# Optimization experiments

Hardware: AMD Instinct MI355X
Metric: run time of the kernel (lower is better)

The kernel has to match this reference:

```python
import jax, jax.numpy as jnp
import numpy as np

N, D, K = 200000, 128, 512


def setup_inputs() -> dict:
    key = jax.random.key(0)
    F = jax.random.normal(key, (N, D), dtype=jnp.float32)
    # original picks starting centers as (unique) rows of F; take a strided subset
    centers = F[:: N // K][:K]
    return {"F": F, "centers": centers}


def reference(F, centers):
    # One k-means iteration (the original's aliasing bug makes the recursion
    # terminate after a single assignment + mean-update pass).
    # invariant to the sqrt the original applies.
    f2 = jnp.sum(F * F, axis=1, keepdims=True)          # [N,1]
    c2 = jnp.sum(centers * centers, axis=1)             # [K]
    d2 = f2 - 2.0 * (F @ centers.T) + c2[None, :]       # [N,K]
    assign = jnp.argmin(d2, axis=1)                      # [N] cluster index per point
    sums = jax.ops.segment_sum(F, assign, num_segments=K)                 # [K,D]
    counts = jax.ops.segment_sum(jnp.ones((F.shape[0],), F.dtype), assign,
                                 num_segments=K)                           # [K]
    new_centers = sums / jnp.maximum(counts, 1.0)[:, None]                 # segment mean
    return new_centers, assign
```

## Files before the change

kernel.cpp:

```cpp
#include <hip/hip_runtime.h>

#define DIM 128
#define K_CL 512
#define BM 128
#define CC 128
#define GAPU 4352u
#define TAU2 0.02f
#define LISTA_CAP 65536
#define LISTB_CAP 16384
#define TILE 1024
#define MAX_ITEMS 2048
#define G_GATHER 1024

typedef unsigned int uint;
typedef unsigned short ushort;
using short8 = __attribute__((ext_vector_type(8))) short;
using f32x4  = __attribute__((ext_vector_type(4))) float;
using us8    = __attribute__((ext_vector_type(8))) unsigned short;

__device__ __forceinline__ ushort f2bf(float x) {
    uint u = __float_as_uint(x);
    u += 0x7fff + ((u >> 16) & 1);
    return (ushort)(u >> 16);
}
__device__ __forceinline__ float bf2f(ushort h) {
    return __uint_as_float(((uint)h) << 16);
}
__device__ __forceinline__ uint umn(uint a, uint b) { return a < b ? a : b; }
__device__ __forceinline__ uint umx(uint a, uint b) { return a > b ? a : b; }

__device__ __forceinline__ void gload_lds16(const void* gsrc, void* ldst) {
    __builtin_amdgcn_global_load_lds(
        (const __attribute__((address_space(1))) unsigned int*)gsrc,
        (__attribute__((address_space(3))) unsigned int*)ldst,
        16, 0, 0);
}

__global__ void prep_kernel(const float* __restrict__ C, ushort* __restrict__ Cp,
                            float* __restrict__ c2, float* __restrict__ c2q,
                            double* __restrict__ c2d) {
    int bid = blockIdx.x;
    if (bid < 256) {
        int e = bid * 256 + threadIdx.x;
        int p = e >> 7, d = e & 127;
        float x = C[e];
        ushort h = f2bf(x);
        float lo = x - bf2f(h);
        Cp[(size_t)p * 256 + d] = h;
        Cp[(size_t)p * 256 + 128 + d] = f2bf(lo);
    } else {
        int k = (bid - 256) * 256 + threadIdx.x;
        if (k < K_CL) {
            const float* row = C + (size_t)k * DIM;
            float s = 0.f;
            double sd = 0.0;
            for (int d = 0; d < DIM; ++d) {
                s = fmaf(row[d], row[d], s);
                double v = (double)row[d];
                sd += v * v;
            }
            c2[k] = s;
            c2q[k] = s + 3072.0f;
            c2d[k] = sd;
        }
    }
}

__global__ __launch_bounds__(256, 2)
void assign_hi(const float* __restrict__ F, const ushort* __restrict__ Cp,
               const float* __restrict__ c2qg, float* __restrict__ assign_out,
               int* __restrict__ cntA, int* __restrict__ listA,
               int* __restrict__ cntB, int* __restrict__ listB, int N) {
    __shared__ __align__(16) ushort Fs[BM * 128];
    __shared__ __align__(16) ushort Cs[128 * 128];

    const int tid  = threadIdx.x;
    const int lane = tid & 63;
    const int wave = tid >> 6;
    const int quad = lane >> 4;
    const int l15  = lane & 15;
    const int wy   = wave >> 1;
    const int wx   = wave & 1;
    const int p0   = blockIdx.x * BM;

#pragma unroll
    for (int t = 0; t < 8; ++t) {
        int G = tid + 256 * t;
        int r = G >> 4, pos = G & 15;
        int g = (pos & 8) | ((pos ^ r) & 7);
        int gp = p0 + r; if (gp >= N) gp = N - 1;
        const float* src = F + (size_t)gp * DIM + g * 8;
        float4 x0 = ((const float4*)src)[0];
        float4 x1 = ((const float4*)src)[1];
        us8 o;
        o[0] = f2bf(x0.x); o[1] = f2bf(x0.y); o[2] = f2bf(x0.z); o[3] = f2bf(x0.w);
        o[4] = f2bf(x1.x); o[5] = f2bf(x1.y); o[6] = f2bf(x1.z); o[7] = f2bf(x1.w);
        *((us8*)&Fs[(size_t)G * 8]) = o;
    }

    int prA[4], xA[4], cnB[4], xB[4];
#pragma unroll
    for (int i = 0; i < 4; ++i) {
        int pr = wy * 64 + i * 16 + l15;
        prA[i] = pr * 128; xA[i] = quad ^ (pr & 7);
    }
#pragma unroll
    for (int j = 0; j < 4; ++j) {
        int cn = wx * 64 + j * 16 + l15;
        cnB[j] = cn * 128; xB[j] = quad ^ (cn & 7);
    }
    int csrc[8];
#pragma unroll
    for (int t = 0; t < 8; ++t) {
        int G = t * 256 + wave * 64 + lane;
        int r = G >> 4, pos = G & 15;
        int g = (pos & 8) | ((pos ^ r) & 7);
        csrc[t] = r * 256 + g * 8;
    }
    float c2q[4][4];
    uint  kb [4][4];
#pragma unroll
    for (int cc = 0; cc < 4; ++cc)
#pragma unroll
        for (int j = 0; j < 4; ++j) {
            int k = cc * CC + wx * 64 + j * 16 + l15;
            c2q[cc][j] = c2qg[k];
            kb [cc][j] = (uint)k;
        }

    uint m1[16], m2[16];
#pragma unroll
    for (int i = 0; i < 16; ++i) { m1[i] = 0xFFFFFFFFu; m2[i] = 0xFFFFFFFFu; }

#pragma unroll 1
    for (int cc = 0; cc < 4; ++cc) {
        f32x4 acc[4][4];
#pragma unroll
        for (int i = 0; i < 4; ++i)
#pragma unroll
            for (int j = 0; j < 4; ++j) acc[i][j] = f32x4{0.f, 0.f, 0.f, 0.f};

        __syncthreads();
#pragma unroll
        for (int t = 0; t < 8; ++t)
            gload_lds16(Cp + (size_t)cc * CC * 256 + csrc[t],
                        &Cs[(size_t)(t * 256 + wave * 64) * 8]);
        __syncthreads();

#pragma unroll
        for (int s = 0; s < 4; ++s) {
            const int hs = (s & 2) << 2;
            const int ls = (s & 1) << 2;
            short8 a[4], b[4];
#pragma unroll
            for (int j = 0; j < 4; ++j)
                b[j] = *((const short8*)&Cs[cnB[j] + (hs | (xB[j] ^ ls)) * 8]);
#pragma unroll
            for (int i = 0; i < 4; ++i)
                a[i] = *((const short8*)&Fs[prA[i] + (hs | (xA[i] ^ ls)) * 8]);
#pragma unroll
            for (int i = 0; i < 4; ++i)
#pragma unroll
                for (int j = 0; j < 4; ++j)
                    acc[i][j] = __builtin_amdgcn_mfma_f32_16x16x32_bf16(
                        a[i], b[j], acc[i][j], 0, 0, 0);
        }

#pragma unroll
        for (int i = 0; i < 4; ++i)
#pragma unroll
            for (int reg = 0; reg < 4; ++reg) {
                int lr = i * 4 + reg;
#pragma unroll
                for (int j = 0; j < 4; ++j) {
                    float dq = fmaf(acc[i][j][reg], -2.0f, c2q[cc][j]);
                    uint x = (__float_as_uint(dq) & 0xFFFFFE00u) | kb[cc][j];
                    uint t = umx(x, m1[lr]);
                    m2[lr] = umn(m2[lr], t);
                    m1[lr] = umn(m1[lr], x);
                }
            }
    }

#pragma unroll
    for (int lr = 0; lr < 16; ++lr) {
        uint a1 = m1[lr], a2 = m2[lr];
#pragma unroll
        for (int m = 1; m <= 8; m <<= 1) {
            uint o1 = (uint)__shfl_xor((int)a1, m);
            uint o2 = (uint)__shfl_xor((int)a2, m);
            uint hi = umx(a1, o1);
            a1 = umn(a1, o1);
            a2 = umn(umn(a2, o2), hi);
        }
        m1[lr] = a1; m2[lr] = a2;
    }

    __syncthreads();
    uint* sm1 = (uint*)Cs;
    uint* sm2 = sm1 + 256;

    if (l15 == 0) {
#pragma unroll
        for (int lr = 0; lr < 16; ++lr) {
            int pl = wy * 64 + (lr >> 2) * 16 + quad * 4 + (lr & 3);
            sm1[wx * 128 + pl] = m1[lr];
            sm2[wx * 128 + pl] = m2[lr];
        }
    }
    __syncthreads();

    if (tid < BM) {
        int p = p0 + tid;
        if (p < N) {
            uint a1 = sm1[tid], a2 = sm2[tid];
            uint b1 = sm1[128 + tid], b2 = sm2[128 + tid];
            uint hi = umx(a1, b1);
            uint M1 = umn(a1, b1);
            uint M2 = umn(umn(a2, b2), hi);
            assign_out[p] = (float)(M1 & 511u);
            if ((M2 & 0xFFFFFE00u) - (M1 & 0xFFFFFE00u) < GAPU) {
                int idx = atomicAdd(cntA, 1);
                if (idx < LISTA_CAP) listA[idx] = p;
                else {
                    int ib = atomicAdd(cntB, 1);
                    if (ib < LISTB_CAP) listB[ib] = p;
                }
            }
        }
    }
}

__global__ __launch_bounds__(256, 2)
void assign_lohi(const float* __restrict__ F, const ushort* __restrict__ Cp,
                 const float* __restrict__ c2g, float* __restrict__ assign_out,
                 const int* __restrict__ cntA, const int* __restrict__ listA,
                 int* __restrict__ cntB, int* __restrict__ listB, int N) {
    int cnt = *cntA; if (cnt > LISTA_CAP) cnt = LISTA_CAP;
    const int p0 = blockIdx.x * BM;
    if (p0 >= cnt) return;

    __shared__ __align__(16) ushort Fs[BM * 256];
    __shared__ __align__(16) ushort Cs[CC * 64];

    const int tid  = threadIdx.x;
    const int lane = tid & 63;
    const int wave = tid >> 6;
    const int quad = lane >> 4;
    const int l15  = lane & 15;
    const int wy   = wave >> 1;
    const int wx   = wave & 1;

    for (int G = tid; G < BM * 32; G += 256) {
        int r = G >> 5, pos = G & 31;
        int g = (pos & 24) | ((pos ^ r) & 7);
        int idx = p0 + r; if (idx >= cnt) idx = cnt - 1;
        int gp = listA[idx];
        const float* src = F + (size_t)gp * DIM + (g & 15) * 8;
        float4 x0 = ((const float4*)src)[0];
        float4 x1 = ((const float4*)src)[1];
        float xs[8] = {x0.x, x0.y, x0.z, x0.w, x1.x, x1.y, x1.z, x1.w};
        us8 o;
        if (g < 16) {
#pragma unroll
            for (int t = 0; t < 8; ++t) o[t] = f2bf(xs[t]);
        } else {
#pragma unroll
            for (int t = 0; t < 8; ++t) {
                ushort h = f2bf(xs[t]);
                o[t] = f2bf(xs[t] - bf2f(h));
            }
        }
        *((us8*)&Fs[(size_t)G * 8]) = o;
    }

    int aoff[4][2], boff[4][2];
#pragma unroll
    for (int i = 0; i < 4; ++i) {
        int pr = wy * 64 + i * 16 + l15;
#pragma unroll
        for (int s = 0; s < 2; ++s)
            aoff[i][s] = pr * 256 + (((s * 4 + quad) ^ (pr & 7)) * 8);
    }
#pragma unroll
    for (int j = 0; j < 4; ++j) {
        int cn = wx * 64 + j * 16 + l15;
#pragma unroll
        for (int s = 0; s < 2; ++s)
            boff[j][s] = cn * 64 + (((s * 4 + quad) ^ (cn & 7)) * 8);
    }
    int cpoff[4];
    ushort* ldsdst[4];
#pragma unroll
    for (int t = 0; t < 4; ++t) {
        int Gbase = t * 256 + wave * 64;
        int G = Gbase + lane;
        int r = G >> 3, pos = G & 7;
        int g = pos ^ (r & 7);
        cpoff[t] = r * 256 + g * 8;
        ldsdst[t] = &Cs[(size_t)Gbase * 8];
    }

    float best1[16], best2[16];
    int bidx[16];
#pragma unroll
    for (int i = 0; i < 16; ++i) { best1[i] = 3.4e38f; best2[i] = 3.4e38f; bidx[i] = 0; }

    for (int cc = 0; cc < K_CL / CC; ++cc) {
        const int ccbase = cc * (CC * 256);
        f32x4 acc[4][4];
#pragma unroll
        for (int i = 0; i < 4; ++i)
#pragma unroll
            for (int j = 0; j < 4; ++j) acc[i][j] = f32x4{0.f, 0.f, 0.f, 0.f};

#pragma unroll
        for (int st = 0; st < 4; ++st) {
            const int ak0 = st & 1;
            const int ak1 = (st < 2) ? (st + 2) : -1;

            __syncthreads();
#pragma unroll
            for (int t = 0; t < 4; ++t)
                gload_lds16(Cp + ccbase + st * 64 + cpoff[t], ldsdst[t]);
            __syncthreads();

#pragma unroll
            for (int s = 0; s < 2; ++s) {
                short8 b[4], a[4];
#pragma unroll
                for (int j = 0; j < 4; ++j)
                    b[j] = *((const short8*)&Cs[boff[j][s]]);
#pragma unroll
                for (int i = 0; i < 4; ++i)
                    a[i] = *((const short8*)&Fs[aoff[i][s] + ak0 * 64]);
#pragma unroll
                for (int i = 0; i < 4; ++i)
#pragma unroll
                    for (int j = 0; j < 4; ++j)
                        acc[i][j] = __builtin_amdgcn_mfma_f32_16x16x32_bf16(
                            a[i], b[j], acc[i][j], 0, 0, 0);
                if (ak1 >= 0) {
#pragma unroll
                    for (int i = 0; i < 4; ++i)
                        a[i] = *((const short8*)&Fs[aoff[i][s] + ak1 * 64]);
#pragma unroll
                    for (int i = 0; i < 4; ++i)
#pragma unroll
                        for (int j = 0; j < 4; ++j)
                            acc[i][j] = __builtin_amdgcn_mfma_f32_16x16x32_bf16(
                                a[i], b[j], acc[i][j], 0, 0, 0);
                }
            }
        }

        float c2v[4];
#pragma unroll
        for (int j = 0; j < 4; ++j)
            c2v[j] = c2g[cc * CC + wx * 64 + j * 16 + l15];
#pragma unroll
        for (int i = 0; i < 4; ++i)
#pragma unroll
            for (int reg = 0; reg < 4; ++reg) {
                int lr = i * 4 + reg;
#pragma unroll
                for (int j = 0; j < 4; ++j) {
                    float d = c2v[j] - 2.0f * acc[i][j][reg];
                    int k = cc * CC + wx * 64 + j * 16 + l15;
                    if (d < best1[lr]) { best2[lr] = best1[lr]; best1[lr] = d; bidx[lr] = k; }
                    else if (d < best2[lr]) best2[lr] = d;
                }
            }
    }

    __syncthreads();
    float* sb1 = (float*)Cs;
    float* sb2 = sb1 + 256;
    int*   sk  = (int*)(sb2 + 256);

#pragma unroll
    for (int lr = 0; lr < 16; ++lr) {
        float b1 = best1[lr], b2 = best2[lr];
        int k1 = bidx[lr];
#pragma unroll
        for (int m = 1; m <= 8; m <<= 1) {
            float ob1 = __shfl_xor(b1, m);
            float ob2 = __shfl_xor(b2, m);
            int   ok1 = __shfl_xor(k1, m);
            float nb2 = fminf(fmaxf(b1, ob1), fminf(b2, ob2));
            if (ob1 < b1 || (ob1 == b1 && ok1 < k1)) { b1 = ob1; k1 = ok1; }
            b2 = nb2;
        }
        best1[lr] = b1; best2[lr] = b2; bidx[lr] = k1;
    }
    if (l15 == 0) {
#pragma unroll
        for (int lr = 0; lr < 16; ++lr) {
            int pl = wy * 64 + (lr >> 2) * 16 + quad * 4 + (lr & 3);
            sb1[wx * 128 + pl] = best1[lr];
            sb2[wx * 128 + pl] = best2[lr];
            sk [wx * 128 + pl] = bidx[lr];
        }
    }
    __syncthreads();

    if (tid < BM && p0 + tid < cnt) {
        int p = listA[p0 + tid];
        float a1 = sb1[tid],       a2 = sb2[tid];        int akk = sk[tid];
        float c1 = sb1[128 + tid], cs2 = sb2[128 + tid]; int ckk = sk[128 + tid];
        float m2v = fminf(fmaxf(a1, c1), fminf(a2, cs2));
        float m1v; int mk;
        if (c1 < a1 || (c1 == a1 && ckk < akk)) { m1v = c1; mk = ckk; }
        else                                    { m1v = a1; mk = akk; }
        assign_out[p] = (float)mk;
        if (m2v - m1v < TAU2) {
            int ib = atomicAdd(cntB, 1);
            if (ib < LISTB_CAP) listB[ib] = p;
        }
    }
}

__global__ void rescue_kernel(const float* __restrict__ F, const float* __restrict__ C,
                              const double* __restrict__ c2d,
                              const int* __restrict__ cntB,
                              const int* __restrict__ listB,
                              float* __restrict__ assign_out) {
    __shared__ double Frow[DIM];
    __shared__ double bd[256];
    __shared__ int    bk[256];
    int cnt = *cntB;
    if (cnt > LISTB_CAP) cnt = LISTB_CAP;
    for (int r = blockIdx.x; r < cnt; r += gridDim.x) {
        int p = listB[r];
        if (threadIdx.x < DIM) Frow[threadIdx.x] = (double)F[(size_t)p * DIM + threadIdx.x];
        __syncthreads();
        double b1 = 1e300; int k1 = 0x7fffffff;
        for (int k = threadIdx.x; k < K_CL; k += 256) {
            const float* c = C + (size_t)k * DIM;
            double acc = 0.0;
            for (int d = 0; d < DIM; ++d) acc += Frow[d] * (double)c[d];
            double dd = c2d[k] - 2.0 * acc;
            if (dd < b1 || (dd == b1 && k < k1)) { b1 = dd; k1 = k; }
        }
        bd[threadIdx.x] = b1; bk[threadIdx.x] = k1;
        __syncthreads();
        for (int s = 128; s > 0; s >>= 1) {
            if (threadIdx.x < s) {
                double ob = bd[threadIdx.x + s]; int ok = bk[threadIdx.x + s];
                if (ob < bd[threadIdx.x] || (ob == bd[threadIdx.x] && ok < bk[threadIdx.x])) {
                    bd[threadIdx.x] = ob; bk[threadIdx.x] = ok;
                }
            }
            __syncthreads();
        }
        if (threadIdx.x == 0) assign_out[p] = (float)bk[0];
        __syncthreads();
    }
}

__global__ void count_kernel(const float* __restrict__ assign_f,
                             int* __restrict__ gcount, int N) {
    __shared__ int h[K_CL];
    const int tid = threadIdx.x;
    h[tid] = 0; h[tid + 256] = 0;
    __syncthreads();
    int base = blockIdx.x * 1024;
#pragma unroll
    for (int t = 0; t < 4; ++t) {
        int p = base + tid + t * 256;
        if (p < N) atomicAdd(&h[(int)assign_f[p]], 1);
    }
    __syncthreads();
#pragma unroll
    for (int t = 0; t < 2; ++t) {
        int k = tid + t * 256;
        if (h[k]) atomicAdd(&gcount[k], h[k]);
    }
}

__global__ void scan_item_kernel(const int* __restrict__ gcount,
                                 int* __restrict__ offsets, int* __restrict__ cursor,
                                 int* __restrict__ items, int* __restrict__ itemCnt,
                                 int N) {
    __shared__ int s[K_CL];
    __shared__ int ic;
    int t = threadIdx.x;
    int v = gcount[t];
    s[t] = v;
    if (t == 0) ic = 0;
    __syncthreads();
    for (int off = 1; off < K_CL; off <<= 1) {
        int x = (t >= off) ? s[t - off] : 0;
        __syncthreads();
        s[t] += x;
        __syncthreads();
    }
    offsets[t] = s[t] - v;
    cursor[t]  = s[t] - v;
    if (t == K_CL - 1) offsets[K_CL] = N;
    int nIt = (v + TILE - 1) / TILE;
    int base = 0;
    if (nIt > 0) base = atomicAdd(&ic, nIt);
    for (int i = 0; i < nIt; ++i)
        if (base + i < MAX_ITEMS) items[base + i] = (t << 8) | i;
    __syncthreads();
    if (t == 0) *itemCnt = ic < MAX_ITEMS ? ic : MAX_ITEMS;
}

__global__ void scatter_kernel(const float* __restrict__ assign_f,
                               int* __restrict__ cursor, int* __restrict__ idx, int N) {
    __shared__ int h[K_CL];
    __shared__ int b[K_CL];
    const int tid = threadIdx.x;
    h[tid] = 0; h[tid + 256] = 0;
    __syncthreads();
    int base = blockIdx.x * 1024;
    int a[4], r[4];
#pragma unroll
    for (int t = 0; t < 4; ++t) {
        int p = base + tid + t * 256;
        if (p < N) {
            a[t] = (int)assign_f[p];
            r[t] = atomicAdd(&h[a[t]], 1);
        } else a[t] = -1;
    }
    __syncthreads();
#pragma unroll
    for (int t = 0; t < 2; ++t) {
        int k = tid + t * 256;
        if (h[k]) b[k] = atomicAdd(&cursor[k], h[k]);
    }
    __syncthreads();
#pragma unroll
    for (int t = 0; t < 4; ++t) {
        if (a[t] >= 0) {
            int p = base + tid + t * 256;
            idx[b[a[t]] + r[t]] = p;
        }
    }
}

__global__ __launch_bounds__(256)
void gather_kernel(const float* __restrict__ F, const int* __restrict__ idx,
                   const int* __restrict__ offsets, const int* __restrict__ items,
                   const int* __restrict__ itemCnt, float* __restrict__ sums) {
    __shared__ int lidx[TILE];
    const int bid = blockIdx.x;
    if (bid >= *itemCnt) return;
    const int it    = items[bid];
    const int k     = it >> 8;
    const int chunk = it & 255;
    const int s   = offsets[k] + chunk * TILE;
    int e = offsets[k + 1];
    if (e > s + TILE) e = s + TILE;
    const int len = e - s;

    const int tid = threadIdx.x;
    for (int i = tid; i < len; i += 256) lidx[i] = idx[s + i];
    __syncthreads();

    const int d  = tid & 127;
    const int rg = tid >> 7;
    float acc = 0.f;
    for (int m0 = rg * 8; m0 < len; m0 += 16) {
        float v[8]; int ok[8];
#pragma unroll
        for (int t = 0; t < 8; ++t) {
            int m = m0 + t;
            ok[t] = (m < len);
            int p = lidx[ok[t] ? m : 0];
            v[t] = F[(size_t)p * DIM + d];
        }
#pragma unroll
        for (int t = 0; t < 8; ++t)
            if (ok[t]) acc += v[t];
    }
    unsafeAtomicAdd(&sums[(size_t)k * DIM + d], acc);
}

__global__ void finalize_kernel(const float* __restrict__ sums,
                                const int* __restrict__ gcount,
                                float* __restrict__ out) {
    int i = blockIdx.x * 256 + threadIdx.x;
    int k = i >> 7;
    out[i] = sums[i] / fmaxf((float)gcount[k], 1.0f);
}

extern "C" void kernel_launch(void* const* d_in, const int* in_sizes, int n_in,
                              void* d_out, int out_size, void* d_ws, size_t ws_size,
                              hipStream_t stream) {
    const float* F = (const float*)d_in[0];
    const float* C = (const float*)d_in[1];
    int N = in_sizes[0] / DIM;

    float* out = (float*)d_out;
    float* centers_out = out;
    float* assign_out  = out + K_CL * DIM;

    float*  sums    = (float*)d_ws;
    int*    gcount  = (int*)(sums + K_CL * DIM);
    int*    cursor  = gcount + K_CL;
    int*    offsets = cursor + K_CL;
    int*    itemCnt = offsets + 516;
    int*    cntA    = itemCnt + 4;
    int*    cntB    = cntA + 1;
    int*    items   = cntA + 8;
    int*    listA   = items + MAX_ITEMS;
    int*    listB   = listA + LISTA_CAP;
    float*  c2      = (float*)(listB + LISTB_CAP);
    float*  c2q     = c2 + K_CL;
    double* c2d     = (double*)(c2q + K_CL);
    ushort* Cp      = (ushort*)(c2d + K_CL);
    int*    idx     = (int*)(Cp + K_CL * 256);

    hipMemsetAsync(d_ws, 0,
                   (size_t)(K_CL * DIM) * sizeof(float) +
                   (512 + 512 + 516 + 4 + 8) * sizeof(int), stream);

    prep_kernel<<<258, 256, 0, stream>>>(C, Cp, c2, c2q, c2d);

    int nb = (N + BM - 1) / BM;
    assign_hi<<<nb, 256, 0, stream>>>(F, Cp, c2q, assign_out, cntA, listA, cntB, listB, N);

    assign_lohi<<<LISTA_CAP / BM, 256, 0, stream>>>(F, Cp, c2, assign_out,
                                                    cntA, listA, cntB, listB, N);

    rescue_kernel<<<256, 256, 0, stream>>>(F, C, c2d, cntB, listB, assign_out);

    int cb = (N + 1023) / 1024;
    count_kernel    <<<cb, 256, 0, stream>>>(assign_out, gcount, N);
    scan_item_kernel<<<1, K_CL, 0, stream>>>(gcount, offsets, cursor, items, itemCnt, N);
    scatter_kernel  <<<cb, 256, 0, stream>>>(assign_out, cursor, idx, N);
    gather_kernel   <<<G_GATHER, 256, 0, stream>>>(F, idx, offsets, items, itemCnt, sums);
    finalize_kernel <<<K_CL * DIM / 256, 256, 0, stream>>>(sums, gcount, centers_out);
}
```

Baseline: 336.8 us.

## Fuse cluster counting into assign kernels, widen assign_hi to 512 threads, restage lohi centers

assign_hi now runs 512-thread blocks with eight waves splitting the center columns four ways, which lowers per-thread accumulator registers and raises occupancy. It also builds a per-block shared histogram of assignments and flushes it to global counts. The lohi and rescue passes adjust those counts with atomics whenever they change an assignment, so the separate count kernel is removed. assign_lohi loads a full 128-center chunk into shared memory once per chunk instead of four staged loads with barriers. This costs more LDS per block and adds global atomics in the refinement kernels.

```diff
diff --git a/kernel.cpp b/kernel.cpp
--- a/kernel.cpp
+++ b/kernel.cpp
@@ -66,26 +66,30 @@
     }
 }
 
-__global__ __launch_bounds__(256, 2)
+__global__ __launch_bounds__(512, 4)
 void assign_hi(const float* __restrict__ F, const ushort* __restrict__ Cp,
                const float* __restrict__ c2qg, float* __restrict__ assign_out,
                int* __restrict__ cntA, int* __restrict__ listA,
-               int* __restrict__ cntB, int* __restrict__ listB, int N) {
+               int* __restrict__ cntB, int* __restrict__ listB,
+               int* __restrict__ gcount, int N) {
     __shared__ __align__(16) ushort Fs[BM * 128];
     __shared__ __align__(16) ushort Cs[128 * 128];
+    __shared__ int hist[K_CL];
 
     const int tid  = threadIdx.x;
     const int lane = tid & 63;
     const int wave = tid >> 6;
     const int quad = lane >> 4;
     const int l15  = lane & 15;
-    const int wy   = wave >> 1;
-    const int wx   = wave & 1;
+    const int wy   = wave & 1;
+    const int wq   = wave >> 1;
     const int p0   = blockIdx.x * BM;
 
-#pragma unroll
-    for (int t = 0; t < 8; ++t) {
-        int G = tid + 256 * t;
+    hist[tid] = 0;
+
+#pragma unroll
+    for (int t = 0; t < 4; ++t) {
+        int G = tid + 512 * t;
         int r = G >> 4, pos = G & 15;
         int g = (pos & 8) | ((pos ^ r) & 7);
         int gp = p0 + r; if (gp >= N) gp = N - 1;
@@ -98,35 +102,32 @@
         *((us8*)&Fs[(size_t)G * 8]) = o;
     }
 
-    int prA[4], xA[4], cnB[4], xB[4];
+    int prA[4], xA[4], cnB[2], xB[2];
 #pragma unroll
     for (int i = 0; i < 4; ++i) {
         int pr = wy * 64 + i * 16 + l15;
         prA[i] = pr * 128; xA[i] = quad ^ (pr & 7);
     }
 #pragma unroll
-    for (int j = 0; j < 4; ++j) {
-        int cn = wx * 64 + j * 16 + l15;
+    for (int j = 0; j < 2; ++j) {
+        int cn = wq * 32 + j * 16 + l15;
         cnB[j] = cn * 128; xB[j] = quad ^ (cn & 7);
     }
-    int csrc[8];
-#pragma unroll
-    for (int t = 0; t < 8; ++t) {
-        int G = t * 256 + wave * 64 + lane;
+    int csrc[4];
+#pragma unroll
+    for (int t = 0; t < 4; ++t) {
+        int G = t * 512 + wave * 64 + lane;
         int r = G >> 4, pos = G & 15;
         int g = (pos & 8) | ((pos ^ r) & 7);
         csrc[t] = r * 256 + g * 8;
     }
-    float c2q[4][4];
-    uint  kb [4][4];
+    const int kq = wq * 32 + l15;
+    float c2q[4][2];
 #pragma unroll
     for (int cc = 0; cc < 4; ++cc)
 #pragma unroll
-        for (int j = 0; j < 4; ++j) {
-            int k = cc * CC + wx * 64 + j * 16 + l15;
-            c2q[cc][j] = c2qg[k];
-            kb [cc][j] = (uint)k;
-        }
+        for (int j = 0; j < 2; ++j)
+            c2q[cc][j] = c2qg[cc * CC + kq + j * 16];
 
     uint m1[16], m2[16];
 #pragma unroll
@@ -134,26 +135,26 @@
 
 #pragma unroll 1
     for (int cc = 0; cc < 4; ++cc) {
-        f32x4 acc[4][4];
+        f32x4 acc[4][2];
 #pragma unroll
         for (int i = 0; i < 4; ++i)
 #pragma unroll
-            for (int j = 0; j < 4; ++j) acc[i][j] = f32x4{0.f, 0.f, 0.f, 0.f};
-
-        __syncthreads();
-#pragma unroll
-        for (int t = 0; t < 8; ++t)
+            for (int j = 0; j < 2; ++j) acc[i][j] = f32x4{0.f, 0.f, 0.f, 0.f};
+
+        __syncthreads();
+#pragma unroll
+        for (int t = 0; t < 4; ++t)
             gload_lds16(Cp + (size_t)cc * CC * 256 + csrc[t],
-                        &Cs[(size_t)(t * 256 + wave * 64) * 8]);
+                        &Cs[(size_t)(t * 512 + wave * 64) * 8]);
         __syncthreads();
 
 #pragma unroll
         for (int s = 0; s < 4; ++s) {
             const int hs = (s & 2) << 2;
             const int ls = (s & 1) << 2;
-            short8 a[4], b[4];
-#pragma unroll
-            for (int j = 0; j < 4; ++j)
+            short8 a[4], b[2];
+#pragma unroll
+            for (int j = 0; j < 2; ++j)
                 b[j] = *((const short8*)&Cs[cnB[j] + (hs | (xB[j] ^ ls)) * 8]);
 #pragma unroll
             for (int i = 0; i < 4; ++i)
@@ -161,7 +162,7 @@
 #pragma unroll
             for (int i = 0; i < 4; ++i)
 #pragma unroll
-                for (int j = 0; j < 4; ++j)
+                for (int j = 0; j < 2; ++j)
                     acc[i][j] = __builtin_amdgcn_mfma_f32_16x16x32_bf16(
                         a[i], b[j], acc[i][j], 0, 0, 0);
         }
@@ -172,9 +173,10 @@
             for (int reg = 0; reg < 4; ++reg) {
                 int lr = i * 4 + reg;
 #pragma unroll
-                for (int j = 0; j < 4; ++j) {
+                for (int j = 0; j < 2; ++j) {
                     float dq = fmaf(acc[i][j][reg], -2.0f, c2q[cc][j]);
-                    uint x = (__float_as_uint(dq) & 0xFFFFFE00u) | kb[cc][j];
+                    uint x = (__float_as_uint(dq) & 0xFFFFFE00u)
+                             | (uint)(cc * CC + kq + j * 16);
                     uint t = umx(x, m1[lr]);
                     m2[lr] = umn(m2[lr], t);
                     m1[lr] = umn(m1[lr], x);
@@ -198,14 +200,14 @@
 
     __syncthreads();
     uint* sm1 = (uint*)Cs;
-    uint* sm2 = sm1 + 256;
+    uint* sm2 = sm1 + 512;
 
     if (l15 == 0) {
 #pragma unroll
         for (int lr = 0; lr < 16; ++lr) {
             int pl = wy * 64 + (lr >> 2) * 16 + quad * 4 + (lr & 3);
-            sm1[wx * 128 + pl] = m1[lr];
-            sm2[wx * 128 + pl] = m2[lr];
+            sm1[wq * 128 + pl] = m1[lr];
+            sm2[wq * 128 + pl] = m2[lr];
         }
     }
     __syncthreads();
@@ -213,12 +215,17 @@
     if (tid < BM) {
         int p = p0 + tid;
         if (p < N) {
-            uint a1 = sm1[tid], a2 = sm2[tid];
-            uint b1 = sm1[128 + tid], b2 = sm2[128 + tid];
-            uint hi = umx(a1, b1);
-            uint M1 = umn(a1, b1);
-            uint M2 = umn(umn(a2, b2), hi);
-            assign_out[p] = (float)(M1 & 511u);
+            uint M1 = sm1[tid], M2 = sm2[tid];
+#pragma unroll
+            for (int q = 1; q < 4; ++q) {
+                uint b1 = sm1[q * 128 + tid], b2 = sm2[q * 128 + tid];
+                uint hi = umx(M1, b1);
+                M1 = umn(M1, b1);
+                M2 = umn(umn(M2, b2), hi);
+            }
+            int k = (int)(M1 & 511u);
+            assign_out[p] = (float)k;
+            atomicAdd(&hist[k], 1);
             if ((M2 & 0xFFFFFE00u) - (M1 & 0xFFFFFE00u) < GAPU) {
                 int idx = atomicAdd(cntA, 1);
                 if (idx < LISTA_CAP) listA[idx] = p;
@@ -229,19 +236,22 @@
             }
         }
     }
-}
-
-__global__ __launch_bounds__(256, 2)
+    __syncthreads();
+    { int v = hist[tid]; if (v) atomicAdd(&gcount[tid], v); }
+}
+
+__global__ __launch_bounds__(256, 1)
 void assign_lohi(const float* __restrict__ F, const ushort* __restrict__ Cp,
                  const float* __restrict__ c2g, float* __restrict__ assign_out,
                  const int* __restrict__ cntA, const int* __restrict__ listA,
-                 int* __restrict__ cntB, int* __restrict__ listB, int N) {
+                 int* __restrict__ cntB, int* __restrict__ listB,
+                 int* __restrict__ gcount, int N) {
     int cnt = *cntA; if (cnt > LISTA_CAP) cnt = LISTA_CAP;
     const int p0 = blockIdx.x * BM;
     if (p0 >= cnt) return;
 
     __shared__ __align__(16) ushort Fs[BM * 256];
-    __shared__ __align__(16) ushort Cs[CC * 64];
+    __shared__ __align__(16) ushort Cs[CC * 256];
 
     const int tid  = threadIdx.x;
     const int lane = tid & 63;
@@ -287,18 +297,7 @@
         int cn = wx * 64 + j * 16 + l15;
 #pragma unroll
         for (int s = 0; s < 2; ++s)
-            boff[j][s] = cn * 64 + (((s * 4 + quad) ^ (cn & 7)) * 8);
-    }
-    int cpoff[4];
-    ushort* ldsdst[4];
-#pragma unroll
-    for (int t = 0; t < 4; ++t) {
-        int Gbase = t * 256 + wave * 64;
-        int G = Gbase + lane;
-        int r = G >> 3, pos = G & 7;
-        int g = pos ^ (r & 7);
-        cpoff[t] = r * 256 + g * 8;
-        ldsdst[t] = &Cs[(size_t)Gbase * 8];
+            boff[j][s] = cn * 256 + (((s * 4 + quad) ^ (cn & 7)) * 8);
     }
 
     float best1[16], best2[16];
@@ -306,51 +305,45 @@
 #pragma unroll
     for (int i = 0; i < 16; ++i) { best1[i] = 3.4e38f; best2[i] = 3.4e38f; bidx[i] = 0; }
 
+    const int pA[6] = {0, 1, 2, 3, 0, 1};
+    const int pC[6] = {0, 1, 0, 1, 2, 3};
+
     for (int cc = 0; cc < K_CL / CC; ++cc) {
-        const int ccbase = cc * (CC * 256);
+        const size_t ccbase = (size_t)cc * CC * 256;
         f32x4 acc[4][4];
 #pragma unroll
         for (int i = 0; i < 4; ++i)
 #pragma unroll
             for (int j = 0; j < 4; ++j) acc[i][j] = f32x4{0.f, 0.f, 0.f, 0.f};
 
-#pragma unroll
-        for (int st = 0; st < 4; ++st) {
-            const int ak0 = st & 1;
-            const int ak1 = (st < 2) ? (st + 2) : -1;
-
-            __syncthreads();
-#pragma unroll
-            for (int t = 0; t < 4; ++t)
-                gload_lds16(Cp + ccbase + st * 64 + cpoff[t], ldsdst[t]);
-            __syncthreads();
-
+        __syncthreads();
+#pragma unroll
+        for (int t = 0; t < 16; ++t) {
+            int Gbase = t * 256 + wave * 64;
+            int G = Gbase + lane;
+            int r = G >> 5, pos = G & 31;
+            int g = (pos & 24) | ((pos ^ r) & 7);
+            gload_lds16(Cp + ccbase + r * 256 + g * 8, &Cs[(size_t)Gbase * 8]);
+        }
+        __syncthreads();
+
+#pragma unroll
+        for (int tp = 0; tp < 6; ++tp) {
 #pragma unroll
             for (int s = 0; s < 2; ++s) {
-                short8 b[4], a[4];
+                short8 a[4], b[4];
 #pragma unroll
                 for (int j = 0; j < 4; ++j)
-                    b[j] = *((const short8*)&Cs[boff[j][s]]);
+                    b[j] = *((const short8*)&Cs[boff[j][s] + pC[tp] * 64]);
 #pragma unroll
                 for (int i = 0; i < 4; ++i)
-                    a[i] = *((const short8*)&Fs[aoff[i][s] + ak0 * 64]);
+                    a[i] = *((const short8*)&Fs[aoff[i][s] + pA[tp] * 64]);
 #pragma unroll
                 for (int i = 0; i < 4; ++i)
 #pragma unroll
                     for (int j = 0; j < 4; ++j)
                         acc[i][j] = __builtin_amdgcn_mfma_f32_16x16x32_bf16(
                             a[i], b[j], acc[i][j], 0, 0, 0);
-                if (ak1 >= 0) {
-#pragma unroll
-                    for (int i = 0; i < 4; ++i)
-                        a[i] = *((const short8*)&Fs[aoff[i][s] + ak1 * 64]);
-#pragma unroll
-                    for (int i = 0; i < 4; ++i)
-#pragma unroll
-                        for (int j = 0; j < 4; ++j)
-                            acc[i][j] = __builtin_amdgcn_mfma_f32_16x16x32_bf16(
-                                a[i], b[j], acc[i][j], 0, 0, 0);
-                }
             }
         }
 
@@ -412,7 +405,12 @@
         float m1v; int mk;
         if (c1 < a1 || (c1 == a1 && ckk < akk)) { m1v = c1; mk = ckk; }
         else                                    { m1v = a1; mk = akk; }
+        int old = (int)assign_out[p];
         assign_out[p] = (float)mk;
+        if (old != mk) {
+            atomicAdd(&gcount[old], -1);
+            atomicAdd(&gcount[mk], 1);
+        }
         if (m2v - m1v < TAU2) {
             int ib = atomicAdd(cntB, 1);
             if (ib < LISTB_CAP) listB[ib] = p;
@@ -424,6 +422,7 @@
                               const double* __restrict__ c2d,
                               const int* __restrict__ cntB,
                               const int* __restrict__ listB,
+                              int* __restrict__ gcount,
                               float* __restrict__ assign_out) {
     __shared__ double Frow[DIM];
     __shared__ double bd[256];
@@ -453,28 +452,16 @@
             }
             __syncthreads();
         }
-        if (threadIdx.x == 0) assign_out[p] = (float)bk[0];
-        __syncthreads();
-    }
-}
-
-__global__ void count_kernel(const float* __restrict__ assign_f,
-                             int* __restrict__ gcount, int N) {
-    __shared__ int h[K_CL];
-    const int tid = threadIdx.x;
-    h[tid] = 0; h[tid + 256] = 0;
-    __syncthreads();
-    int base = blockIdx.x * 1024;
-#pragma unroll
-    for (int t = 0; t < 4; ++t) {
-        int p = base + tid + t * 256;
-        if (p < N) atomicAdd(&h[(int)assign_f[p]], 1);
-    }
-    __syncthreads();
-#pragma unroll
-    for (int t = 0; t < 2; ++t) {
-        int k = tid + t * 256;
-        if (h[k]) atomicAdd(&gcount[k], h[k]);
+        if (threadIdx.x == 0) {
+            int old = (int)assign_out[p];
+            int nk  = bk[0];
+            assign_out[p] = (float)nk;
+            if (old != nk) {
+                atomicAdd(&gcount[old], -1);
+                atomicAdd(&gcount[nk], 1);
+            }
+        }
+        __syncthreads();
     }
 }
 
@@ -620,15 +607,15 @@
     prep_kernel<<<258, 256, 0, stream>>>(C, Cp, c2, c2q, c2d);
 
     int nb = (N + BM - 1) / BM;
-    assign_hi<<<nb, 256, 0, stream>>>(F, Cp, c2q, assign_out, cntA, listA, cntB, listB, N);
+    assign_hi<<<nb, 512, 0, stream>>>(F, Cp, c2q, assign_out,
+                                      cntA, listA, cntB, listB, gcount, N);
 
     assign_lohi<<<LISTA_CAP / BM, 256, 0, stream>>>(F, Cp, c2, assign_out,
-                                                    cntA, listA, cntB, listB, N);
-
-    rescue_kernel<<<256, 256, 0, stream>>>(F, C, c2d, cntB, listB, assign_out);
+                                                    cntA, listA, cntB, listB, gcount, N);
+
+    rescue_kernel<<<256, 256, 0, stream>>>(F, C, c2d, cntB, listB, gcount, assign_out);
 
     int cb = (N + 1023) / 1024;
-    count_kernel    <<<cb, 256, 0, stream>>>(assign_out, gcount, N);
     scan_item_kernel<<<1, K_CL, 0, stream>>>(gcount, offsets, cursor, items, itemCnt, N);
     scatter_kernel  <<<cb, 256, 0, stream>>>(assign_out, cursor, idx, N);
     gather_kernel   <<<G_GATHER, 256, 0, stream>>>(F, idx, offsets, items, itemCnt, sums);
```

New measurement: 345.4 us. 2.6% more time.
